# Optimization experiments

Measured on AMD Instinct MI355X. Metric: run time of the kernel, lower is better.

The kernel has to match this reference:

```python
import jax, jax.numpy as jnp
import numpy as np

B, F, C, NS, P, N = 256, 2048, 16384, 65536, 8, 32
T, W_BU, W_H, P_MARGIN, N_MARGIN = 1.0, 1.0, 10.0, 0.1, 0.1


def setup_inputs() -> dict:
    key = jax.random.key(0)
    ks = jax.random.split(key, 8)
    inputs = jax.random.normal(ks[0], (B, F), jnp.float32)
    targets = jax.random.randint(ks[1], (B,), 0, C)
    # batch global indices: unique (original .item() assumes a single match)
    indexs = jax.random.permutation(ks[2], NS)[:B].astype(jnp.int64) if False else jax.random.permutation(ks[2], jnp.arange(NS))[:B]
    # positive candidates drawn from in-batch indices so they are found in `indexs`
    pos_sel = jax.random.randint(ks[3], (B, P), 0, B)
    ppairs = indexs[pos_sel]
    # negative candidates: arbitrary global indices (mostly not in batch)
    npairs = jax.random.randint(ks[4], (B, N), 0, NS)
    all_label_to_clusterid = jax.random.randint(ks[5], (NS,), 0, C)
    V = jax.random.normal(ks[6], (C, F), jnp.float32)
    V = V / jnp.linalg.norm(V, axis=1, keepdims=True)  # bank rows are L2-normalized by the update rule
    return {"inputs": inputs, "targets": targets, "ppairs": ppairs, "npairs": npairs,
            "indexs": indexs, "all_label_to_clusterid": all_label_to_clusterid, "V": V, "epoch": 1}


def _forward(inputs, targets, ppairs, npairs, indexs, all_label_to_clusterid, V, epoch):
    # Exclusive branch: logits against the memory bank (V treated as constant)
    outputs = (inputs @ V.T) * T  # [B, C]
    logp = jax.nn.log_softmax(outputs, axis=1)
    bu_loss = -jnp.mean(jnp.take_along_axis(logp, targets[:, None], axis=1))

    # ms_loss (use_prior=True, use_table=True)
    ni = inputs / jnp.linalg.norm(inputs, axis=1, keepdims=True)
    sims = ni @ ni.T          # [B, B]
    tsims = ni @ V.T          # [B, C]

    # positives found in the batch: (ppair == indexs).nonzero()
    mp = ppairs[:, :, None] == indexs[None, None, :]        # [B, P, B]
    found_p = jnp.any(mp, axis=2)
    idx_p = jnp.argmax(mp, axis=2)
    psim_b = jnp.take_along_axis(sims, idx_p, axis=1)       # [B, P]
    mask_pb = found_p & (ppairs >= 0)
    # table positive: tsims[i, target] appended if nonzero
    tp = jnp.take_along_axis(tsims, targets[:, None], axis=1)  # [B, 1]
    mask_tp = tp != 0
    psims = jnp.concatenate([psim_b, tp], axis=1)           # [B, P+1]
    pmask = jnp.concatenate([mask_pb, mask_tp], axis=1)

    # negatives found in the batch
    mn = npairs[:, :, None] == indexs[None, None, :]        # [B, N, B]
    found_n = jnp.any(mn, axis=2)
    idx_n = jnp.argmax(mn, axis=2)
    nsim_b = jnp.take_along_axis(sims, idx_n, axis=1)       # [B, N]
    mask_nb = found_n & (npairs >= 0)
    # table negative appended for EVERY npair (indent level in original): tsims[i, clusterid[npair]]
    ncid = all_label_to_clusterid[jnp.clip(npairs, 0, None)]
    tn = jnp.take_along_axis(tsims, ncid, axis=1)           # [B, N]
    mask_tn = (npairs >= 0) & (tn != 0)
    nsims = jnp.concatenate([nsim_b, tn], axis=1)           # [B, 2N]
    nmask = jnp.concatenate([mask_nb, mask_tn], axis=1)

    # thresholds: max(nsims) or -3 (+p_margin); min(psims) or 3 (-n_margin)
    p_thrd = jnp.where(jnp.any(nmask, 1), jnp.max(jnp.where(nmask, nsims, -jnp.inf), 1), -3.0) + P_MARGIN
    n_thrd = jnp.where(jnp.any(pmask, 1), jnp.min(jnp.where(pmask, psims, jnp.inf), 1), 3.0) - N_MARGIN

    hp = pmask & (psims < p_thrd[:, None])
    hn = nmask & (nsims > n_thrd[:, None]) & (nsims < 0.999999)

    hp_sum = jnp.sum(jnp.where(hp, jnp.exp(-2.0 * (psims - 0.5)), 0.0))
    hn_sum = jnp.sum(jnp.where(hn, jnp.exp(50.0 * (nsims - 0.5)), 0.0))
    hp_loss = jnp.where(jnp.any(hp), 0.5 * jnp.log1p(hp_sum), 0.0)
    hn_loss = jnp.where(jnp.any(hn), (1.0 / 50.0) * jnp.log1p(hn_sum), 0.0)
    # original builds hpsims/hnsims with torch.tensor(...), which DETACHES them
    h_loss = jax.lax.stop_gradient(hp_loss + hn_loss)

    loss = W_BU * bu_loss + W_H * h_loss
    return loss, outputs


def reference(inputs, targets, ppairs, npairs, indexs, all_label_to_clusterid, V, epoch):
    return _forward(inputs, targets, ppairs, npairs, indexs, all_label_to_clusterid, V, epoch)
```

## Files before the change

### kernel.cpp

```cpp
#include <hip/hip_runtime.h>
#include <hip/hip_bf16.h>
#include <math.h>

#define B_SZ 256
#define F_SZ 2048
#define C_SZ 16384
#define P_SZ 8
#define N_SZ 32
#define NTILE 512

typedef __bf16 bf16x8 __attribute__((ext_vector_type(8)));
typedef float f32x4 __attribute__((ext_vector_type(4)));
typedef unsigned short us8 __attribute__((ext_vector_type(8)));
typedef unsigned short us4 __attribute__((ext_vector_type(4)));

typedef __attribute__((address_space(3))) unsigned int lds_u32;
typedef __attribute__((address_space(1))) const unsigned int glb_u32;

__device__ __forceinline__ unsigned short f2bf(float x) {
    union { float f; unsigned int u; } v; v.f = x;
    unsigned int r = v.u + 0x7FFFu + ((v.u >> 16) & 1u);
    return (unsigned short)(r >> 16);
}

__global__ __launch_bounds__(256) void prep_kernel(const float* __restrict__ inputs,
                                                   unsigned short* __restrict__ Abf,
                                                   float* __restrict__ norms) {
    const int row = blockIdx.x;
    const int tid = threadIdx.x;
    const float* rp = inputs + (size_t)row * F_SZ + tid * 8;
    float4 v0 = *(const float4*)(rp);
    float4 v1 = *(const float4*)(rp + 4);
    us8 o;
    o[0]=f2bf(v0.x); o[1]=f2bf(v0.y); o[2]=f2bf(v0.z); o[3]=f2bf(v0.w);
    o[4]=f2bf(v1.x); o[5]=f2bf(v1.y); o[6]=f2bf(v1.z); o[7]=f2bf(v1.w);
    *(us8*)(Abf + (size_t)row * F_SZ + tid * 8) = o;
    float ss = v0.x*v0.x + v0.y*v0.y + v0.z*v0.z + v0.w*v0.w
             + v1.x*v1.x + v1.y*v1.y + v1.z*v1.z + v1.w*v1.w;
    __shared__ float red[256];
    red[tid] = ss; __syncthreads();
    for (int s = 128; s > 0; s >>= 1) { if (tid < s) red[tid] += red[tid+s]; __syncthreads(); }
    if (tid == 0) norms[row] = sqrtf(red[0]);
}

#define BM 256
#define BN 64
#define BK 32
#define BPAD 40
#define KITERS (F_SZ / BK)

__global__ __launch_bounds__(1024) void gemm_kernel(const unsigned short* __restrict__ Abf,
                                                    const float* __restrict__ V,
                                                    float* __restrict__ Cout,
                                                    float* __restrict__ pmax,
                                                    float* __restrict__ psum) {
    __shared__ unsigned short As[2][4 * 256 * 8];
    __shared__ unsigned short Bs[2][BN * BPAD];

    const int tid = threadIdx.x;
    const int lane = tid & 63;
    const int wid = tid >> 6;
    const int wrow = wid & 7, wcol = wid >> 3;
    const int q = lane >> 4, l16 = lane & 15;
    const int bn0 = blockIdx.x * BN;

    f32x4 acc[2][2];
    #pragma unroll
    for (int i = 0; i < 2; i++)
        #pragma unroll
        for (int j = 0; j < 2; j++) acc[i][j] = (f32x4){0.f, 0.f, 0.f, 0.f};

    const int arow = tid & 255, achk = tid >> 8;
    const unsigned short* AgBase = Abf + (size_t)arow * F_SZ + achk * 8;

    const int brow = tid >> 3, bseg = tid & 7;
    const float* BgBase = V + (size_t)(bn0 + brow) * F_SZ + bseg * 4;
    unsigned short* Bsd0 = &Bs[0][brow * BPAD + bseg * 4];
    unsigned short* Bsd1 = &Bs[1][brow * BPAD + bseg * 4];

    float4 bv;

    auto issueA = [&](int buf, int k0) {
        __builtin_amdgcn_global_load_lds((glb_u32*)(AgBase + k0),
                                         (lds_u32*)&As[buf][(size_t)tid * 8], 16, 0, 0);
    };
    auto loadB = [&](int k0) {
        if (tid < 512) bv = *(const float4*)(BgBase + k0);
    };
    auto writeB = [&](unsigned short* dst) {
        if (tid < 512) {
            us4 w;
            w[0]=f2bf(bv.x); w[1]=f2bf(bv.y); w[2]=f2bf(bv.z); w[3]=f2bf(bv.w);
            *(us4*)dst = w;
        }
    };

    issueA(0, 0);
    loadB(0);
    writeB(Bsd0);
    __syncthreads();

    for (int it = 0; it < KITERS; ++it) {
        const int cur = it & 1;
        const bool more = (it + 1) < KITERS;
        if (more) {
            issueA(cur ^ 1, (it + 1) * BK);
            loadB((it + 1) * BK);
        }
        bf16x8 af[2], bfv[2];
        #pragma unroll
        for (int mi = 0; mi < 2; ++mi) {
            const int row = wrow * 32 + mi * 16 + l16;
            af[mi] = *(const bf16x8*)&As[cur][(size_t)(q * 256 + row) * 8];
        }
        #pragma unroll
        for (int ni = 0; ni < 2; ++ni) {
            const int col = wcol * 32 + ni * 16 + l16;
            bfv[ni] = *(const bf16x8*)&Bs[cur][col * BPAD + q * 8];
        }
        #pragma unroll
        for (int mi = 0; mi < 2; ++mi)
            #pragma unroll
            for (int ni = 0; ni < 2; ++ni)
                acc[mi][ni] = __builtin_amdgcn_mfma_f32_16x16x32_bf16(af[mi], bfv[ni], acc[mi][ni], 0, 0, 0);
        if (more) writeB(cur ? Bsd0 : Bsd1);
        __syncthreads();
    }

    #pragma unroll
    for (int mi = 0; mi < 2; ++mi) {
        const int r0 = wrow * 32 + mi * 16 + q * 4;
        #pragma unroll
        for (int ni = 0; ni < 2; ++ni) {
            const int c0 = bn0 + wcol * 32 + ni * 16 + l16;
            #pragma unroll
            for (int r = 0; r < 4; ++r)
                Cout[(size_t)(r0 + r) * C_SZ + c0] = acc[mi][ni][r];
        }
    }

    const int tileIdx = blockIdx.x * 2 + wcol;
    #pragma unroll
    for (int mi = 0; mi < 2; ++mi) {
        #pragma unroll
        for (int r = 0; r < 4; ++r) {
            float mloc = fmaxf(acc[mi][0][r], acc[mi][1][r]);
            #pragma unroll
            for (int off = 1; off < 16; off <<= 1)
                mloc = fmaxf(mloc, __shfl_xor(mloc, off, 64));
            float sloc = __expf(acc[mi][0][r] - mloc) + __expf(acc[mi][1][r] - mloc);
            #pragma unroll
            for (int off = 1; off < 16; off <<= 1)
                sloc += __shfl_xor(sloc, off, 64);
            if (l16 == 0) {
                const int grow = wrow * 32 + mi * 16 + q * 4 + r;
                pmax[grow * NTILE + tileIdx] = mloc;
                psum[grow * NTILE + tileIdx] = sloc;
            }
        }
    }
}

__global__ __launch_bounds__(256) void softmax_combine_kernel(
    const float* __restrict__ pmax, const float* __restrict__ psum,
    const float* __restrict__ outputs, const int* __restrict__ targets,
    float* __restrict__ bu_part)
{
    const int row = blockIdx.x;
    const int tid = threadIdx.x;
    __shared__ float rm[256], rs[256];
    float m1 = pmax[row * NTILE + tid],       s1 = psum[row * NTILE + tid];
    float m2 = pmax[row * NTILE + tid + 256], s2 = psum[row * NTILE + tid + 256];
    float nm = fmaxf(m1, m2);
    rm[tid] = nm;
    rs[tid] = s1 * __expf(m1 - nm) + s2 * __expf(m2 - nm);
    __syncthreads();
    for (int s = 128; s > 0; s >>= 1) {
        if (tid < s) {
            float a = rm[tid], sa = rs[tid];
            float b = rm[tid + s], sb = rs[tid + s];
            float nn = fmaxf(a, b);
            rs[tid] = sa * __expf(a - nn) + sb * __expf(b - nn);
            rm[tid] = nn;
        }
        __syncthreads();
    }
    if (tid == 0) {
        float logZ = rm[0] + logf(rs[0]);
        bu_part[row] = -(outputs[(size_t)row * C_SZ + targets[row]] - logZ);
    }
}

__global__ __launch_bounds__(256) void pairs_kernel(
    const float* __restrict__ inputs, const int* __restrict__ targets,
    const int* __restrict__ ppairs, const int* __restrict__ npairs,
    const int* __restrict__ indexs, const int* __restrict__ cluster,
    const float* __restrict__ outputs, const float* __restrict__ norms,
    float* __restrict__ hp_part, float* __restrict__ hn_part,
    int* __restrict__ flag_part)
{
    const int i = blockIdx.x;
    const int tid = threadIdx.x;
    __shared__ int idxbuf[B_SZ];
    __shared__ int pj[P_SZ];
    __shared__ int nj[N_SZ];
    __shared__ float simp[P_SZ];
    __shared__ float simn[N_SZ];
    __shared__ float tnv[N_SZ];
    __shared__ float s_tp;

    idxbuf[tid] = indexs[tid];
    __syncthreads();

    const float* row = outputs + (size_t)i * C_SZ;
    const float ni_norm = norms[i];

    if (tid < P_SZ) {
        int pp = ppairs[i * P_SZ + tid];
        int f = -1;
        if (pp >= 0) for (int j = 0; j < B_SZ; j++) if (idxbuf[j] == pp) { f = j; break; }
        pj[tid] = f;
    } else if (tid < P_SZ + N_SZ) {
        int t = tid - P_SZ;
        int np = npairs[i * N_SZ + t];
        int f = -1;
        if (np >= 0) for (int j = 0; j < B_SZ; j++) if (idxbuf[j] == np) { f = j; break; }
        nj[t] = f;
        int cid = cluster[np < 0 ? 0 : np];
        tnv[t] = row[cid] / ni_norm;
    }
    if (tid == P_SZ + N_SZ) s_tp = row[targets[i]] / ni_norm;
    __syncthreads();

    const int lane = tid & 63, wv = tid >> 6;
    for (int qq = wv; qq < P_SZ + N_SZ; qq += 4) {
        int j = (qq < P_SZ) ? pj[qq] : nj[qq - P_SZ];
        float s = 0.f;
        if (j >= 0) {
            const float* xi = inputs + (size_t)i * F_SZ;
            const float* xj = inputs + (size_t)j * F_SZ;
            float d = 0.f;
            for (int k = lane; k < F_SZ; k += 64) d += xi[k] * xj[k];
            for (int off = 32; off > 0; off >>= 1) d += __shfl_down(d, off);
            s = d / (ni_norm * norms[j]);
        }
        if (lane == 0) { if (qq < P_SZ) simp[qq] = s; else simn[qq - P_SZ] = s; }
    }
    __syncthreads();

    if (tid == 0) {
        float psims[P_SZ + 1]; bool pmask[P_SZ + 1];
        for (int p = 0; p < P_SZ; p++) {
            int pp = ppairs[i * P_SZ + p];
            pmask[p] = (pj[p] >= 0) && (pp >= 0);
            psims[p] = simp[p];
        }
        psims[P_SZ] = s_tp; pmask[P_SZ] = (s_tp != 0.0f);

        float nsims[2 * N_SZ]; bool nmask[2 * N_SZ];
        for (int t = 0; t < N_SZ; t++) {
            int np = npairs[i * N_SZ + t];
            nmask[t] = (nj[t] >= 0) && (np >= 0);
            nsims[t] = simn[t];
            nsims[N_SZ + t] = tnv[t];
            nmask[N_SZ + t] = (np >= 0) && (tnv[t] != 0.0f);
        }
        bool anyp = false, anyn = false;
        float maxn = -INFINITY, minp = INFINITY;
        for (int t = 0; t < 2 * N_SZ; t++) if (nmask[t]) { anyn = true; maxn = fmaxf(maxn, nsims[t]); }
        for (int p = 0; p < P_SZ + 1; p++) if (pmask[p]) { anyp = true; minp = fminf(minp, psims[p]); }
        float p_thrd = (anyn ? maxn : -3.0f) + 0.1f;
        float n_thrd = (anyp ? minp : 3.0f) - 0.1f;
        float hps = 0.f, hns = 0.f; int fl = 0;
        for (int p = 0; p < P_SZ + 1; p++)
            if (pmask[p] && psims[p] < p_thrd) { fl |= 1; hps += expf(-2.0f * (psims[p] - 0.5f)); }
        for (int t = 0; t < 2 * N_SZ; t++)
            if (nmask[t] && nsims[t] > n_thrd && nsims[t] < 0.999999f) { fl |= 2; hns += expf(50.0f * (nsims[t] - 0.5f)); }
        hp_part[i] = hps; hn_part[i] = hns; flag_part[i] = fl;
    }
}

__global__ __launch_bounds__(256) void finalize_kernel(
    const float* __restrict__ bu_part, const float* __restrict__ hp_part,
    const float* __restrict__ hn_part, const int* __restrict__ flag_part,
    float* __restrict__ d_out)
{
    __shared__ float r1[256], r2[256], r3[256];
    __shared__ int rf[256];
    const int tid = threadIdx.x;
    r1[tid] = bu_part[tid]; r2[tid] = hp_part[tid]; r3[tid] = hn_part[tid]; rf[tid] = flag_part[tid];
    __syncthreads();
    for (int s = 128; s > 0; s >>= 1) {
        if (tid < s) { r1[tid] += r1[tid+s]; r2[tid] += r2[tid+s]; r3[tid] += r3[tid+s]; rf[tid] |= rf[tid+s]; }
        __syncthreads();
    }
    if (tid == 0) {
        float bu = r1[0] / (float)B_SZ;
        float hp_loss = (rf[0] & 1) ? 0.5f * log1pf(r2[0]) : 0.0f;
        float hn_loss = (rf[0] & 2) ? (1.0f / 50.0f) * log1pf(r3[0]) : 0.0f;
        d_out[0] = 1.0f * bu + 10.0f * (hp_loss + hn_loss);
    }
}

extern "C" void kernel_launch(void* const* d_in, const int* in_sizes, int n_in,
                              void* d_out, int out_size, void* d_ws, size_t ws_size,
                              hipStream_t stream) {
    const float* inputs  = (const float*)d_in[0];
    const int*   targets = (const int*)d_in[1];
    const int*   ppairs  = (const int*)d_in[2];
    const int*   npairs  = (const int*)d_in[3];
    const int*   indexs  = (const int*)d_in[4];
    const int*   cluster = (const int*)d_in[5];
    const float* V       = (const float*)d_in[6];
    float* out = (float*)d_out;

    char* ws = (char*)d_ws;
    unsigned short* Abf = (unsigned short*)ws;
    float* norms   = (float*)(ws + (size_t)B_SZ * F_SZ * 2);
    float* bu_part = norms + B_SZ;
    float* hp_part = bu_part + B_SZ;
    float* hn_part = hp_part + B_SZ;
    int*   flag_part = (int*)(hn_part + B_SZ);
    float* pmax = (float*)(flag_part + B_SZ);
    float* psum = pmax + (size_t)B_SZ * NTILE;

    prep_kernel<<<B_SZ, 256, 0, stream>>>(inputs, Abf, norms);
    gemm_kernel<<<dim3(C_SZ / BN, 1), 1024, 0, stream>>>(Abf, V, out + 1, pmax, psum);
    softmax_combine_kernel<<<B_SZ, 256, 0, stream>>>(pmax, psum, out + 1, targets, bu_part);
    pairs_kernel<<<B_SZ, 256, 0, stream>>>(inputs, targets, ppairs, npairs, indexs,
                                           cluster, out + 1, norms,
                                           hp_part, hn_part, flag_part);
    finalize_kernel<<<1, 256, 0, stream>>>(bu_part, hp_part, hn_part, flag_part, out);
}
```

Before: 337.1 us.

## Restructure GEMM to 64-row tiles with V streamed directly into registers

The GEMM is retiled so each 512-thread block handles 64 batch rows by 128 columns. The block stages its A slice in LDS in 512-wide K phases, with register prefetch of the next phase. Each wave now loads its V rows straight from global memory into registers, converting to bf16 on the fly, instead of going through a shared B buffer with a barrier every 32-wide K step. Partial softmax statistics are merged per block inside the kernel, which shrinks the pmax/psum arrays and the combine kernel. The likely trade-off is that each V row is now read by four blocks (one per 64-row group), where before one block covered all 256 rows. It also relies on uncoalesced per-lane V loads to hide latency.

```diff
diff --git a/kernel.cpp b/kernel.cpp
--- a/kernel.cpp
+++ b/kernel.cpp
@@ -7,15 +7,11 @@
 #define C_SZ 16384
 #define P_SZ 8
 #define N_SZ 32
-#define NTILE 512
+#define NTILE 128
 
 typedef __bf16 bf16x8 __attribute__((ext_vector_type(8)));
 typedef float f32x4 __attribute__((ext_vector_type(4)));
 typedef unsigned short us8 __attribute__((ext_vector_type(8)));
-typedef unsigned short us4 __attribute__((ext_vector_type(4)));
-
-typedef __attribute__((address_space(3))) unsigned int lds_u32;
-typedef __attribute__((address_space(1))) const unsigned int glb_u32;
 
 __device__ __forceinline__ unsigned short f2bf(float x) {
     union { float f; unsigned int u; } v; v.f = x;
@@ -43,139 +39,133 @@
     if (tid == 0) norms[row] = sqrtf(red[0]);
 }
 
-#define BM 256
-#define BN 64
-#define BK 32
-#define BPAD 40
-#define KITERS (F_SZ / BK)
-
-__global__ __launch_bounds__(1024) void gemm_kernel(const unsigned short* __restrict__ Abf,
-                                                    const float* __restrict__ V,
-                                                    float* __restrict__ Cout,
-                                                    float* __restrict__ pmax,
-                                                    float* __restrict__ psum) {
-    __shared__ unsigned short As[2][4 * 256 * 8];
-    __shared__ unsigned short Bs[2][BN * BPAD];
+#define BMG 64
+#define PHK 512
+#define NPH (F_SZ / PHK)
+#define KCP (PHK / 8)
+#define LDA 520
+
+__global__ __launch_bounds__(512, 4) void gemm_kernel(const unsigned short* __restrict__ Abf,
+                                                      const float* __restrict__ V,
+                                                      float* __restrict__ Cout,
+                                                      float* __restrict__ pmax,
+                                                      float* __restrict__ psum) {
+    __shared__ unsigned short As[KCP * LDA];
+    __shared__ float sm[BMG * 8], ss2[BMG * 8];
 
     const int tid = threadIdx.x;
     const int lane = tid & 63;
-    const int wid = tid >> 6;
-    const int wrow = wid & 7, wcol = wid >> 3;
+    const int wv = tid >> 6;
     const int q = lane >> 4, l16 = lane & 15;
-    const int bn0 = blockIdx.x * BN;
-
-    f32x4 acc[2][2];
+    const int m0 = (blockIdx.x & 3) * BMG;
+    const int slab = blockIdx.x >> 2;
+    const int n0 = slab * 128 + wv * 16;
+
+    f32x4 acc[4];
     #pragma unroll
-    for (int i = 0; i < 2; i++)
+    for (int i = 0; i < 4; i++) acc[i] = (f32x4){0.f, 0.f, 0.f, 0.f};
+
+    const int sr = tid >> 3, sc8 = tid & 7;
+    const unsigned short* AgBase = Abf + (size_t)(m0 + sr) * F_SZ;
+
+    #pragma unroll
+    for (int j = 0; j < 8; ++j) {
+        const int kc = sc8 + 8 * j;
+        us8 v = *(const us8*)(AgBase + kc * 8);
+        *(us8*)&As[kc * LDA + sr * 8] = v;
+    }
+    __syncthreads();
+
+    const float* bvp = V + (size_t)(n0 + l16) * F_SZ + q * 8;
+    us8 areg[8];
+
+    for (int ph = 0; ph < NPH; ++ph) {
+        if (ph + 1 < NPH) {
+            #pragma unroll
+            for (int j = 0; j < 8; ++j) {
+                const int kc = sc8 + 8 * j;
+                areg[j] = *(const us8*)(AgBase + (ph + 1) * PHK + kc * 8);
+            }
+        }
+        #pragma unroll 4
+        for (int ks = 0; ks < 16; ++ks) {
+            const int off = ph * PHK + ks * 32;
+            float4 x0 = *(const float4*)(bvp + off);
+            float4 x1 = *(const float4*)(bvp + off + 4);
+            union { us8 u; bf16x8 b; } cv;
+            cv.u[0]=f2bf(x0.x); cv.u[1]=f2bf(x0.y); cv.u[2]=f2bf(x0.z); cv.u[3]=f2bf(x0.w);
+            cv.u[4]=f2bf(x1.x); cv.u[5]=f2bf(x1.y); cv.u[6]=f2bf(x1.z); cv.u[7]=f2bf(x1.w);
+            const int kc = ks * 4 + q;
+            #pragma unroll
+            for (int mi = 0; mi < 4; ++mi) {
+                bf16x8 af = *(const bf16x8*)&As[kc * LDA + (mi * 16 + l16) * 8];
+                acc[mi] = __builtin_amdgcn_mfma_f32_16x16x32_bf16(af, cv.b, acc[mi], 0, 0, 0);
+            }
+        }
+        __syncthreads();
+        if (ph + 1 < NPH) {
+            #pragma unroll
+            for (int j = 0; j < 8; ++j)
+                *(us8*)&As[(sc8 + 8 * j) * LDA + sr * 8] = areg[j];
+            __syncthreads();
+        }
+    }
+
+    #pragma unroll
+    for (int mi = 0; mi < 4; ++mi) {
+        const int r0 = m0 + mi * 16 + q * 4;
+        const int c0 = n0 + l16;
         #pragma unroll
-        for (int j = 0; j < 2; j++) acc[i][j] = (f32x4){0.f, 0.f, 0.f, 0.f};
-
-    const int arow = tid & 255, achk = tid >> 8;
-    const unsigned short* AgBase = Abf + (size_t)arow * F_SZ + achk * 8;
-
-    const int brow = tid >> 3, bseg = tid & 7;
-    const float* BgBase = V + (size_t)(bn0 + brow) * F_SZ + bseg * 4;
-    unsigned short* Bsd0 = &Bs[0][brow * BPAD + bseg * 4];
-    unsigned short* Bsd1 = &Bs[1][brow * BPAD + bseg * 4];
-
-    float4 bv;
-
-    auto issueA = [&](int buf, int k0) {
-        __builtin_amdgcn_global_load_lds((glb_u32*)(AgBase + k0),
-                                         (lds_u32*)&As[buf][(size_t)tid * 8], 16, 0, 0);
-    };
-    auto loadB = [&](int k0) {
-        if (tid < 512) bv = *(const float4*)(BgBase + k0);
-    };
-    auto writeB = [&](unsigned short* dst) {
-        if (tid < 512) {
-            us4 w;
-            w[0]=f2bf(bv.x); w[1]=f2bf(bv.y); w[2]=f2bf(bv.z); w[3]=f2bf(bv.w);
-            *(us4*)dst = w;
-        }
-    };
-
-    issueA(0, 0);
-    loadB(0);
-    writeB(Bsd0);
-    __syncthreads();
-
-    for (int it = 0; it < KITERS; ++it) {
-        const int cur = it & 1;
-        const bool more = (it + 1) < KITERS;
-        if (more) {
-            issueA(cur ^ 1, (it + 1) * BK);
-            loadB((it + 1) * BK);
-        }
-        bf16x8 af[2], bfv[2];
-        #pragma unroll
-        for (int mi = 0; mi < 2; ++mi) {
-            const int row = wrow * 32 + mi * 16 + l16;
-            af[mi] = *(const bf16x8*)&As[cur][(size_t)(q * 256 + row) * 8];
-        }
-        #pragma unroll
-        for (int ni = 0; ni < 2; ++ni) {
-            const int col = wcol * 32 + ni * 16 + l16;
-            bfv[ni] = *(const bf16x8*)&Bs[cur][col * BPAD + q * 8];
-        }
-        #pragma unroll
-        for (int mi = 0; mi < 2; ++mi)
-            #pragma unroll
-            for (int ni = 0; ni < 2; ++ni)
-                acc[mi][ni] = __builtin_amdgcn_mfma_f32_16x16x32_bf16(af[mi], bfv[ni], acc[mi][ni], 0, 0, 0);
-        if (more) writeB(cur ? Bsd0 : Bsd1);
-        __syncthreads();
+        for (int r = 0; r < 4; ++r)
+            Cout[(size_t)(r0 + r) * C_SZ + c0] = acc[mi][r];
     }
 
     #pragma unroll
-    for (int mi = 0; mi < 2; ++mi) {
-        const int r0 = wrow * 32 + mi * 16 + q * 4;
-        #pragma unroll
-        for (int ni = 0; ni < 2; ++ni) {
-            const int c0 = bn0 + wcol * 32 + ni * 16 + l16;
-            #pragma unroll
-            for (int r = 0; r < 4; ++r)
-                Cout[(size_t)(r0 + r) * C_SZ + c0] = acc[mi][ni][r];
-        }
-    }
-
-    const int tileIdx = blockIdx.x * 2 + wcol;
-    #pragma unroll
-    for (int mi = 0; mi < 2; ++mi) {
+    for (int mi = 0; mi < 4; ++mi) {
         #pragma unroll
         for (int r = 0; r < 4; ++r) {
-            float mloc = fmaxf(acc[mi][0][r], acc[mi][1][r]);
+            float mloc = acc[mi][r];
             #pragma unroll
             for (int off = 1; off < 16; off <<= 1)
                 mloc = fmaxf(mloc, __shfl_xor(mloc, off, 64));
-            float sloc = __expf(acc[mi][0][r] - mloc) + __expf(acc[mi][1][r] - mloc);
+            float sloc = __expf(acc[mi][r] - mloc);
             #pragma unroll
             for (int off = 1; off < 16; off <<= 1)
                 sloc += __shfl_xor(sloc, off, 64);
             if (l16 == 0) {
-                const int grow = wrow * 32 + mi * 16 + q * 4 + r;
-                pmax[grow * NTILE + tileIdx] = mloc;
-                psum[grow * NTILE + tileIdx] = sloc;
+                const int lrow = mi * 16 + q * 4 + r;
+                sm[lrow * 8 + wv] = mloc;
+                ss2[lrow * 8 + wv] = sloc;
             }
         }
     }
-}
-
-__global__ __launch_bounds__(256) void softmax_combine_kernel(
+    __syncthreads();
+    if (tid < BMG) {
+        float m = -INFINITY, s = 0.f;
+        #pragma unroll
+        for (int w = 0; w < 8; ++w) {
+            float m2 = sm[tid * 8 + w], s2 = ss2[tid * 8 + w];
+            float nm = fmaxf(m, m2);
+            s = s * __expf(m - nm) + s2 * __expf(m2 - nm);
+            m = nm;
+        }
+        pmax[(m0 + tid) * NTILE + slab] = m;
+        psum[(m0 + tid) * NTILE + slab] = s;
+    }
+}
+
+__global__ __launch_bounds__(128) void softmax_combine_kernel(
     const float* __restrict__ pmax, const float* __restrict__ psum,
     const float* __restrict__ outputs, const int* __restrict__ targets,
     float* __restrict__ bu_part)
 {
     const int row = blockIdx.x;
     const int tid = threadIdx.x;
-    __shared__ float rm[256], rs[256];
-    float m1 = pmax[row * NTILE + tid],       s1 = psum[row * NTILE + tid];
-    float m2 = pmax[row * NTILE + tid + 256], s2 = psum[row * NTILE + tid + 256];
-    float nm = fmaxf(m1, m2);
-    rm[tid] = nm;
-    rs[tid] = s1 * __expf(m1 - nm) + s2 * __expf(m2 - nm);
-    __syncthreads();
-    for (int s = 128; s > 0; s >>= 1) {
+    __shared__ float rm[128], rs[128];
+    rm[tid] = pmax[row * NTILE + tid];
+    rs[tid] = psum[row * NTILE + tid];
+    __syncthreads();
+    for (int s = 64; s > 0; s >>= 1) {
         if (tid < s) {
             float a = rm[tid], sa = rs[tid];
             float b = rm[tid + s], sb = rs[tid + s];
@@ -325,8 +315,8 @@
     float* psum = pmax + (size_t)B_SZ * NTILE;
 
     prep_kernel<<<B_SZ, 256, 0, stream>>>(inputs, Abf, norms);
-    gemm_kernel<<<dim3(C_SZ / BN, 1), 1024, 0, stream>>>(Abf, V, out + 1, pmax, psum);
-    softmax_combine_kernel<<<B_SZ, 256, 0, stream>>>(pmax, psum, out + 1, targets, bu_part);
+    gemm_kernel<<<512, 512, 0, stream>>>(Abf, V, out + 1, pmax, psum);
+    softmax_combine_kernel<<<B_SZ, 128, 0, stream>>>(pmax, psum, out + 1, targets, bu_part);
     pairs_kernel<<<B_SZ, 256, 0, stream>>>(inputs, targets, ppairs, npairs, indexs,
                                            cluster, out + 1, norms,
                                            hp_part, hn_part, flag_part);
```

After: 372.3 us. +10.4%, slower.
